# Optimization experiments

Hardware: AMD Instinct MI355X
Metric: run time of the kernel (lower is better)

## Reference

```python
import jax, jax.numpy as jnp
import numpy as np

MARGIN = 0.1


def setup_inputs() -> dict:
    key = jax.random.key(0)
    k1, k2 = jax.random.split(key)
    n = 8192
    n_classes = 1024
    sim_mat = jax.random.normal(k1, (n, n), dtype=jnp.float32)
    # ensure every class has at least 2 members: tile class ids then shuffle
    base = jnp.tile(jnp.arange(n_classes, dtype=jnp.int64), n // n_classes)
    targets = jax.random.permutation(k2, base)
    idx = jnp.arange(n, dtype=jnp.int64)
    return {"sim_mat": sim_mat, "targets": targets, "idx": idx}


def reference(sim_mat, targets, idx):
    # rows[i, :] = sim_mat[idx[i], :]  (here idx = arange, but keep general)
    rows = sim_mat[idx]                                   # [n, n]
    same = targets[:, None] == targets[None, :]           # [n, n] label match
    self_mask = idx[:, None] == jnp.arange(sim_mat.shape[1])[None, :]
    pos_mask = same & ~self_mask                          # positives excl. self
    neg_mask = ~same                                      # negatives
    big = jnp.asarray(jnp.finfo(rows.dtype).max, rows.dtype)
    pos = jnp.min(jnp.where(pos_mask, rows, big), axis=1)   # hardest positive
    neg = jnp.max(jnp.where(neg_mask, rows, -big), axis=1)  # hardest negative
    loss = jnp.maximum(neg - pos + MARGIN, 0.0)
    return jnp.mean(loss)
```

## Files before the change

### kernel.cpp

```cpp
#include <hip/hip_runtime.h>
#include <float.h>

#define MARGIN 0.1f

typedef float  fx4 __attribute__((ext_vector_type(4)));
typedef int    ix4 __attribute__((ext_vector_type(4)));

__device__ __forceinline__ void acc_elem(float s, int tg, int ti, int j, int self_col,
                                         float& pmin, float& nmax) {
    const bool same = (tg == ti);
    const float pv = (same && j != self_col) ? s : FLT_MAX;
    const float nv = same ? -FLT_MAX : s;
    pmin = fminf(pmin, pv);
    nmax = fmaxf(nmax, nv);
}

__device__ __forceinline__ void acc_vec4(fx4 s, ix4 tg, int ti, int j0, int self_col,
                                         float& pmin, float& nmax) {
    acc_elem(s.x, tg.x, ti, j0 + 0, self_col, pmin, nmax);
    acc_elem(s.y, tg.y, ti, j0 + 1, self_col, pmin, nmax);
    acc_elem(s.z, tg.z, ti, j0 + 2, self_col, pmin, nmax);
    acc_elem(s.w, tg.w, ti, j0 + 3, self_col, pmin, nmax);
}

__global__ __launch_bounds__(256) void triplet_row_kernel(
    const float* __restrict__ sim,
    const int* __restrict__ targets,
    const int* __restrict__ idx,
    float* __restrict__ row_loss,
    int n)
{
    const int i = blockIdx.x;
    const int r = idx[i];
    const int self_col = r;
    const int ti = targets[i];

    const fx4* __restrict__ row4 = (const fx4*)(sim + (long long)r * (long long)n);
    const ix4* __restrict__ tgt4 = (const ix4*)targets;

    float pmin = FLT_MAX;
    float nmax = -FLT_MAX;

    const int tid = threadIdx.x;
    const int nvec = n >> 2;

    int v = tid;
    for (; v + 768 < nvec; v += 1024) {
        const fx4 s0 = __builtin_nontemporal_load(&row4[v]);
        const fx4 s1 = __builtin_nontemporal_load(&row4[v + 256]);
        const fx4 s2 = __builtin_nontemporal_load(&row4[v + 512]);
        const fx4 s3 = __builtin_nontemporal_load(&row4[v + 768]);
        const ix4 t0 = tgt4[v];
        const ix4 t1 = tgt4[v + 256];
        const ix4 t2 = tgt4[v + 512];
        const ix4 t3 = tgt4[v + 768];
        acc_vec4(s0, t0, ti, (v) << 2, self_col, pmin, nmax);
        acc_vec4(s1, t1, ti, (v + 256) << 2, self_col, pmin, nmax);
        acc_vec4(s2, t2, ti, (v + 512) << 2, self_col, pmin, nmax);
        acc_vec4(s3, t3, ti, (v + 768) << 2, self_col, pmin, nmax);
    }
    for (; v < nvec; v += 256) {
        const fx4 s = __builtin_nontemporal_load(&row4[v]);
        const ix4 tg = tgt4[v];
        acc_vec4(s, tg, ti, v << 2, self_col, pmin, nmax);
    }
    const float* __restrict__ row = (const float*)row4;
    for (int j = (nvec << 2) + tid; j < n; j += 256) {
        acc_elem(row[j], targets[j], ti, j, self_col, pmin, nmax);
    }

    #pragma unroll
    for (int off = 32; off > 0; off >>= 1) {
        pmin = fminf(pmin, __shfl_down(pmin, off));
        nmax = fmaxf(nmax, __shfl_down(nmax, off));
    }

    __shared__ float s_pmin[4];
    __shared__ float s_nmax[4];
    const int wave = tid >> 6;
    const int lane = tid & 63;
    if (lane == 0) {
        s_pmin[wave] = pmin;
        s_nmax[wave] = nmax;
    }
    __syncthreads();
    if (tid == 0) {
        float p = fminf(fminf(s_pmin[0], s_pmin[1]), fminf(s_pmin[2], s_pmin[3]));
        float q = fmaxf(fmaxf(s_nmax[0], s_nmax[1]), fmaxf(s_nmax[2], s_nmax[3]));
        row_loss[i] = fmaxf(q - p + MARGIN, 0.0f);
    }
}

__global__ __launch_bounds__(1024) void mean_reduce_kernel(
    const float* __restrict__ row_loss,
    float* __restrict__ out,
    int n)
{
    const int tid = threadIdx.x;
    float acc = 0.0f;
    for (int i = tid; i < n; i += 1024) acc += row_loss[i];

    #pragma unroll
    for (int off = 32; off > 0; off >>= 1)
        acc += __shfl_down(acc, off);

    __shared__ float s_sum[16];
    const int wave = tid >> 6;
    const int lane = tid & 63;
    if (lane == 0) s_sum[wave] = acc;
    __syncthreads();
    if (tid == 0) {
        float total = 0.0f;
        #pragma unroll
        for (int w = 0; w < 16; ++w) total += s_sum[w];
        out[0] = total / (float)n;
    }
}

extern "C" void kernel_launch(void* const* d_in, const int* in_sizes, int n_in,
                              void* d_out, int out_size, void* d_ws, size_t ws_size,
                              hipStream_t stream) {
    const float* sim = (const float*)d_in[0];
    const int* targets = (const int*)d_in[1];
    const int* idx = (const int*)d_in[2];
    const int n = in_sizes[2];

    float* row_loss = (float*)d_ws;
    float* out = (float*)d_out;

    triplet_row_kernel<<<n, 256, 0, stream>>>(sim, targets, idx, row_loss, n);
    mean_reduce_kernel<<<1, 1024, 0, stream>>>(row_loss, out, n);
}
```

Baseline: 336.5 us.

## Process four rows per block and keep target labels in registers

Each 512-thread block now handles four consecutive rows instead of one row per 256-thread block. Each thread loads its slice of the target labels into registers once and reuses it for all four rows. Per-wave partial min/max values go to shared memory, and a single barrier finalizes the four row losses. This cuts redundant target reads and per-block overhead. The trade-off is a fixed column coverage of KCHUNK*BLK*4 elements, so larger n would silently skip columns, and less memory parallelism per row.

```diff
diff --git a/kernel.cpp b/kernel.cpp
--- a/kernel.cpp
+++ b/kernel.cpp
@@ -1,10 +1,14 @@
 #include <hip/hip_runtime.h>
 #include <float.h>
+#include <limits.h>
 
 #define MARGIN 0.1f
+#define BLK 512
+#define ROWS 4
+#define KCHUNK 4
 
-typedef float  fx4 __attribute__((ext_vector_type(4)));
-typedef int    ix4 __attribute__((ext_vector_type(4)));
+typedef float fx4 __attribute__((ext_vector_type(4)));
+typedef int   ix4 __attribute__((ext_vector_type(4)));
 
 __device__ __forceinline__ void acc_elem(float s, int tg, int ti, int j, int self_col,
                                          float& pmin, float& nmax) {
@@ -23,71 +27,78 @@
     acc_elem(s.w, tg.w, ti, j0 + 3, self_col, pmin, nmax);
 }
 
-__global__ __launch_bounds__(256) void triplet_row_kernel(
+__global__ __launch_bounds__(BLK) void triplet_rows_kernel(
     const float* __restrict__ sim,
     const int* __restrict__ targets,
     const int* __restrict__ idx,
     float* __restrict__ row_loss,
     int n)
 {
-    const int i = blockIdx.x;
-    const int r = idx[i];
-    const int self_col = r;
-    const int ti = targets[i];
-
-    const fx4* __restrict__ row4 = (const fx4*)(sim + (long long)r * (long long)n);
+    const int tid = threadIdx.x;
+    const int nvec = n >> 2;
+    const int i0 = blockIdx.x * ROWS;
     const ix4* __restrict__ tgt4 = (const ix4*)targets;
 
-    float pmin = FLT_MAX;
-    float nmax = -FLT_MAX;
-
-    const int tid = threadIdx.x;
-    const int nvec = n >> 2;
-
-    int v = tid;
-    for (; v + 768 < nvec; v += 1024) {
-        const fx4 s0 = __builtin_nontemporal_load(&row4[v]);
-        const fx4 s1 = __builtin_nontemporal_load(&row4[v + 256]);
-        const fx4 s2 = __builtin_nontemporal_load(&row4[v + 512]);
-        const fx4 s3 = __builtin_nontemporal_load(&row4[v + 768]);
-        const ix4 t0 = tgt4[v];
-        const ix4 t1 = tgt4[v + 256];
-        const ix4 t2 = tgt4[v + 512];
-        const ix4 t3 = tgt4[v + 768];
-        acc_vec4(s0, t0, ti, (v) << 2, self_col, pmin, nmax);
-        acc_vec4(s1, t1, ti, (v + 256) << 2, self_col, pmin, nmax);
-        acc_vec4(s2, t2, ti, (v + 512) << 2, self_col, pmin, nmax);
-        acc_vec4(s3, t3, ti, (v + 768) << 2, self_col, pmin, nmax);
-    }
-    for (; v < nvec; v += 256) {
-        const fx4 s = __builtin_nontemporal_load(&row4[v]);
-        const ix4 tg = tgt4[v];
-        acc_vec4(s, tg, ti, v << 2, self_col, pmin, nmax);
-    }
-    const float* __restrict__ row = (const float*)row4;
-    for (int j = (nvec << 2) + tid; j < n; j += 256) {
-        acc_elem(row[j], targets[j], ti, j, self_col, pmin, nmax);
+    ix4 tg[KCHUNK];
+    int vbase[KCHUNK];
+    #pragma unroll
+    for (int k = 0; k < KCHUNK; ++k) {
+        const int v = tid + k * BLK;
+        vbase[k] = v;
+        if (v < nvec) tg[k] = tgt4[v];
     }
 
+    __shared__ float s_p[ROWS][BLK / 64];
+    __shared__ float s_n[ROWS][BLK / 64];
+
     #pragma unroll
-    for (int off = 32; off > 0; off >>= 1) {
-        pmin = fminf(pmin, __shfl_down(pmin, off));
-        nmax = fmaxf(nmax, __shfl_down(nmax, off));
+    for (int rr = 0; rr < ROWS; ++rr) {
+        const int i = i0 + rr;
+        if (i >= n) break;
+        const int r = idx[i];
+        const int ti = targets[i];
+        const int self_col = r;
+        const fx4* __restrict__ row4 = (const fx4*)(sim + (size_t)r * (size_t)n);
+
+        fx4 s[KCHUNK];
+        #pragma unroll
+        for (int k = 0; k < KCHUNK; ++k)
+            if (vbase[k] < nvec) s[k] = __builtin_nontemporal_load(&row4[vbase[k]]);
+
+        float pmin = FLT_MAX, nmax = -FLT_MAX;
+        #pragma unroll
+        for (int k = 0; k < KCHUNK; ++k)
+            if (vbase[k] < nvec)
+                acc_vec4(s[k], tg[k], ti, vbase[k] << 2, self_col, pmin, nmax);
+
+        for (int j = (nvec << 2) + tid; j < n; j += BLK)
+            acc_elem(sim[(size_t)r * (size_t)n + j], targets[j], ti, j, self_col,
+                     pmin, nmax);
+
+        #pragma unroll
+        for (int off = 32; off > 0; off >>= 1) {
+            pmin = fminf(pmin, __shfl_down(pmin, off));
+            nmax = fmaxf(nmax, __shfl_down(nmax, off));
+        }
+        const int wave = tid >> 6;
+        const int lane = tid & 63;
+        if (lane == 0) { s_p[rr][wave] = pmin; s_n[rr][wave] = nmax; }
     }
 
-    __shared__ float s_pmin[4];
-    __shared__ float s_nmax[4];
-    const int wave = tid >> 6;
-    const int lane = tid & 63;
-    if (lane == 0) {
-        s_pmin[wave] = pmin;
-        s_nmax[wave] = nmax;
-    }
     __syncthreads();
-    if (tid == 0) {
-        float p = fminf(fminf(s_pmin[0], s_pmin[1]), fminf(s_pmin[2], s_pmin[3]));
-        float q = fmaxf(fmaxf(s_nmax[0], s_nmax[1]), fmaxf(s_nmax[2], s_nmax[3]));
-        row_loss[i] = fmaxf(q - p + MARGIN, 0.0f);
+
+    if (tid < ROWS) {
+        const int i = i0 + tid;
+        if (i < n) {
+            float p = s_p[tid][0];
+            float q = s_n[tid][0];
+            #pragma unroll
+            for (int w = 1; w < BLK / 64; ++w) {
+                p = fminf(p, s_p[tid][w]);
+                q = fmaxf(q, s_n[tid][w]);
+            }
+            row_loss[i] = fmaxf(q - p + MARGIN, 0.0f);
+        }
     }
 }
 
@@ -128,6 +139,7 @@
     float* row_loss = (float*)d_ws;
     float* out = (float*)d_out;
 
-    triplet_row_kernel<<<n, 256, 0, stream>>>(sim, targets, idx, row_loss, n);
+    const int grid = (n + ROWS - 1) / ROWS;
+    triplet_rows_kernel<<<grid, BLK, 0, stream>>>(sim, targets, idx, row_loss, n);
     mean_reduce_kernel<<<1, 1024, 0, stream>>>(row_loss, out, n);
 }
```

Result: no change. 335.8 us (-0.2%).
